# Performance work log

Measured on AMD Instinct MI355X. Metric: run time of the kernel, lower is better.

The kernel has to match this reference:

```python
import jax, jax.numpy as jnp
import numpy as np

N = 50000      # nodes
E = 800000     # edges
T = 3          # npass
ED = 64        # embedding_dim
NS = 23        # nshifts (arange(0.8, 3.0+1e-5, 0.1))
MD = NS + ED   # message_dim = 87
H = 200        # hidden width (hardcoded in module)
NMOL = 2048    # number of molecules (segments for final scatter)
RD = ED * (T + 1)  # readout input dim = 256
EPS = 1e-5

SHIFTS = jnp.asarray(np.arange(0.8, 3.0 + 1e-5, 0.1, dtype=np.float32))  # [23]


def setup_inputs() -> dict:
    key = jax.random.key(0)
    ks = jax.random.split(key, 32)
    inp = {
        'z_i': jax.random.randint(ks[0], (N,), 0, 10),
        'edge_index': jax.random.randint(ks[1], (2, E), 0, N),
        'dist_ij': jax.random.uniform(ks[2], (E, 1), dtype=jnp.float32) * 2.2 + 0.8,
        'mol_ind': jnp.sort(jax.random.randint(ks[3], (N,), 0, NMOL)),
        'emb': jax.random.normal(ks[4], (10, ED), dtype=jnp.float32),
        # per-pass update MLP params, stacked over T
        'up_bn_g': jnp.ones((T, MD), jnp.float32),
        'up_bn_b': jnp.zeros((T, MD), jnp.float32),
        'up_w1': jax.random.normal(ks[5], (T, MD, H), jnp.float32) * 0.05,
        'up_b1': jnp.zeros((T, H), jnp.float32),
        'up_w2': jax.random.normal(ks[6], (T, H, H), jnp.float32) * 0.05,
        'up_b2': jnp.zeros((T, H), jnp.float32),
        'up_w3': jax.random.normal(ks[7], (T, H, H), jnp.float32) * 0.05,
        'up_b3': jnp.zeros((T, H), jnp.float32),
        'up_w4': jax.random.normal(ks[8], (T, H, ED), jnp.float32) * 0.05,
        'up_b4': jnp.zeros((T, ED), jnp.float32),
        # readout MLP params
        'ro_bn_g': jnp.ones((RD,), jnp.float32),
        'ro_bn_b': jnp.zeros((RD,), jnp.float32),
        'ro_w1': jax.random.normal(ks[9], (RD, H), jnp.float32) * 0.05,
        'ro_b1': jnp.zeros((H,), jnp.float32),
        'ro_w2': jax.random.normal(ks[10], (H, H), jnp.float32) * 0.05,
        'ro_b2': jnp.zeros((H,), jnp.float32),
        'ro_w3': jax.random.normal(ks[11], (H, H), jnp.float32) * 0.05,
        'ro_b3': jnp.zeros((H,), jnp.float32),
        'ro_w4': jax.random.normal(ks[12], (H, 1), jnp.float32) * 0.05,
        'ro_b4': jnp.zeros((1,), jnp.float32),  # bias filled to 0 in __init__
    }
    return inp


def batchnorm(x, g, b):
    # BatchNorm1d in training mode: batch statistics, biased variance
    mu = jnp.mean(x, axis=0)
    var = jnp.mean(jnp.square(x - mu), axis=0)
    return (x - mu) * jax.lax.rsqrt(var + EPS) * g + b


def mlp(x, g, b, w1, b1, w2, b2, w3, b3, w4, b4):
    x = batchnorm(x, g, b)
    x = jax.nn.relu(x @ w1 + b1)
    x = jax.nn.relu(x @ w2 + b2)
    x = jax.nn.relu(x @ w3 + b3)
    return x @ w4 + b4


def reference(z_i, edge_index, dist_ij, mol_ind, emb,
              up_bn_g, up_bn_b, up_w1, up_b1, up_w2, up_b2, up_w3, up_b3, up_w4, up_b4,
              ro_bn_g, ro_bn_b, ro_w1, ro_b1, ro_w2, ro_b2, ro_w3, ro_b3, ro_w4, ro_b4):
    e_source, e_sink = edge_index[0], edge_index[1]
    rbf_ij = jnp.exp(-jnp.square(dist_ij - SHIFTS[None, :]))  # [E, NS]
    x_i = emb[z_i]                                            # [N, ED]
    x_list = [x_i]
    for t in range(T):
        m_ij = jnp.concatenate([rbf_ij, x_i[e_sink]], axis=1)  # [E, MD] gather
        m_i = jax.ops.segment_sum(m_ij, e_source, num_segments=N)  # scatter-sum
        x_i = x_i + 0.1 * mlp(m_i, up_bn_g[t], up_bn_b[t],
                              up_w1[t], up_b1[t], up_w2[t], up_b2[t],
                              up_w3[t], up_b3[t], up_w4[t], up_b4[t])
        x_list.append(x_i)
    x_all = jnp.concatenate(x_list, axis=1)  # [N, RD]
    y_i = mlp(x_all, ro_bn_g, ro_bn_b, ro_w1, ro_b1, ro_w2, ro_b2, ro_w3, ro_b3, ro_w4, ro_b4)
    y = jax.ops.segment_sum(y_i, mol_ind, num_segments=NMOL)  # [NMOL, 1]
    return y
```

## Files before the change

### kernel.cpp

```cpp
#include <hip/hip_runtime.h>
#include <hip/hip_bf16.h>
#include <type_traits>

#define NN 50000
#define NP 50048
#define EE 800000
#define TT 3
#define ED 64
#define NS 23
#define MD 87
#define HH 200
#define NMOL 2048
#define RD 256

#define SP 216
#define NPB2 512
#define SNB ((NN + 255) / 256)

typedef __attribute__((ext_vector_type(8))) short short8b;
typedef __attribute__((ext_vector_type(4))) short short4b;
typedef __attribute__((ext_vector_type(4))) float f32x4;

__device__ __forceinline__ unsigned short f2bf(float f) {
  unsigned u = __float_as_uint(f);
  return (unsigned short)((u + 0x7fffu + ((u >> 16) & 1u)) >> 16);
}
__device__ __forceinline__ float ubf2f(unsigned short h) {
  return __uint_as_float(((unsigned)h) << 16);
}
__device__ __forceinline__ float bfp2f(unsigned p) {
  return __uint_as_float(p << 16) + __uint_as_float(p & 0xffff0000u);
}
__device__ __forceinline__ unsigned packsplit(float v) {
  unsigned short h = f2bf(v);
  unsigned short l = f2bf(v - ubf2f(h));
  return (unsigned)h | ((unsigned)l << 16);
}

struct WD { const float* src; short* dst; int K, N, Kpad, Npad, T; };
struct WDs { WD d[5]; };

__global__ __launch_bounds__(256) void wprep_kernel(WDs W) {
  WD w = W.d[blockIdx.y];
  int KB = w.Kpad >> 5, NT = w.Npad >> 4;
  int per = w.Npad * w.Kpad;
  int total = w.T * per;
  for (int idx = blockIdx.x * 256 + threadIdx.x; idx < total; idx += gridDim.x * 256) {
    int t = idx / per;
    int r = idx - t * per;
    int e = r & 7, lane = (r >> 3) & 63;
    int blk = r >> 9;
    int kb = blk % KB, tile = blk / KB;
    int ln = lane & 15, quad = lane >> 4;
    int n = tile * 16 + ln, k = kb * 32 + quad * 8 + e;
    float v = 0.f;
    if (k < w.K && n < w.N) v = w.src[((size_t)t * w.K + k) * w.N + n];
    unsigned short h = f2bf(v);
    unsigned short l = f2bf(v - ubf2f(h));
    size_t base = ((size_t)(t * NT + tile) * KB + kb) * 1024;
    w.dst[base + lane * 8 + e] = (short)h;
    w.dst[base + 512 + lane * 8 + e] = (short)l;
  }
}

__global__ __launch_bounds__(256) void wscale_kernel(const float* __restrict__ wsrc,
                                                     const float* __restrict__ na,
                                                     const float* __restrict__ nb,
                                                     const float* __restrict__ bsrc,
                                                     int K, int Kpad,
                                                     short* __restrict__ wsp,
                                                     float* __restrict__ bc) {
  int n = blockIdx.x;
  int k = threadIdx.x;
  int KB = Kpad >> 5;
  int tile = n >> 4, ln = n & 15;
  float contrib = 0.f;
  if (k < Kpad) {
    float v = 0.f;
    if (n < HH && k < K) {
      float w = wsrc[(size_t)k * HH + n];
      v = na[k] * w;
      contrib = nb[k] * w;
    }
    unsigned short h = f2bf(v);
    unsigned short l = f2bf(v - ubf2f(h));
    int kb = k >> 5, quad = (k & 31) >> 3, e = k & 7;
    int lane = quad * 16 + ln;
    size_t base = ((size_t)tile * KB + kb) * 1024;
    wsp[base + lane * 8 + e] = (short)h;
    wsp[base + 512 + lane * 8 + e] = (short)l;
  }
  __shared__ float sh[256];
  sh[k] = contrib;
  __syncthreads();
  for (int off = 128; off > 0; off >>= 1) {
    if (k < off) sh[k] += sh[k + off];
    __syncthreads();
  }
  if (k == 0) bc[n] = (n < HH ? bsrc[n] : 0.f) + sh[0];
}

__global__ __launch_bounds__(256) void emb_kernel(const int* __restrict__ z,
                                                  const float* __restrict__ emb,
                                                  unsigned* __restrict__ xp,
                                                  short* __restrict__ xq,
                                                  short* __restrict__ xqs) {
  int idx = blockIdx.x * 256 + threadIdx.x;
  if (idx >= NN * ED) return;
  int i = idx >> 6, d = idx & 63;
  unsigned pk = packsplit(emb[z[i] * ED + d]);
  xp[(size_t)i * RD + d] = pk;
  short h = (short)(pk & 0xffffu);
  xq[(size_t)i * RD + d] = h;
  xqs[(size_t)i * ED + d] = h;
}

__global__ __launch_bounds__(256) void hist_kernel(const int* __restrict__ src,
                                                   int* __restrict__ deg) {
  int e = blockIdx.x * 256 + threadIdx.x;
  if (e < EE) atomicAdd(&deg[src[e]], 1);
}

__global__ __launch_bounds__(256) void scanA_kernel(const int* __restrict__ deg,
                                                    int* __restrict__ Psum) {
  int i = blockIdx.x * 256 + threadIdx.x;
  int v = (i < NN) ? deg[i] : 0;
#pragma unroll
  for (int off = 32; off > 0; off >>= 1) v += __shfl_down(v, off, 64);
  __shared__ int ws[4];
  if ((threadIdx.x & 63) == 0) ws[threadIdx.x >> 6] = v;
  __syncthreads();
  if (threadIdx.x == 0) Psum[blockIdx.x] = ws[0] + ws[1] + ws[2] + ws[3];
}

__global__ __launch_bounds__(256) void scanB_kernel(const int* __restrict__ Psum,
                                                    int* __restrict__ Poff) {
  __shared__ int sh[256];
  int t = threadIdx.x;
  int v = (t < SNB) ? Psum[t] : 0;
  sh[t] = v;
  __syncthreads();
  for (int off = 1; off < 256; off <<= 1) {
    int u = (t >= off) ? sh[t - off] : 0;
    __syncthreads();
    sh[t] += u;
    __syncthreads();
  }
  if (t < SNB) Poff[t] = sh[t] - v;
}

__global__ __launch_bounds__(256) void scanC_kernel(const int* __restrict__ deg,
                                                    const int* __restrict__ Poff,
                                                    int* __restrict__ offs,
                                                    int* __restrict__ cursor) {
  __shared__ int sh[256];
  int t = threadIdx.x;
  int i = blockIdx.x * 256 + t;
  int v = (i < NN) ? deg[i] : 0;
  sh[t] = v;
  __syncthreads();
  for (int off = 1; off < 256; off <<= 1) {
    int u = (t >= off) ? sh[t - off] : 0;
    __syncthreads();
    sh[t] += u;
    __syncthreads();
  }
  int excl = Poff[blockIdx.x] + sh[t] - v;
  if (i < NN) {
    offs[i] = excl;
    cursor[i] = excl;
    if (i == NN - 1) offs[NN] = excl + v;
  }
}

__global__ __launch_bounds__(256) void scatter_kernel(const int* __restrict__ src,
                                                      const int* __restrict__ snk,
                                                      const float* __restrict__ dist,
                                                      int* __restrict__ cursor,
                                                      int* __restrict__ ssink,
                                                      float* __restrict__ sdist) {
  int e = blockIdx.x * 256 + threadIdx.x;
  if (e >= EE) return;
  int p = atomicAdd(&cursor[src[e]], 1);
  ssink[p] = snk[e];
  sdist[p] = dist[e];
}

template <bool RBF>
__global__ __launch_bounds__(256) void gather_kernel(const int* __restrict__ offs,
                                                     const int* __restrict__ ssink,
                                                     const float* __restrict__ sdist,
                                                     const short* __restrict__ xqs,
                                                     short* __restrict__ mh) {
  int node = blockIdx.x * 4 + (threadIdx.x >> 6);
  int lane = threadIdx.x & 63;
  if (node >= NN) return;
  float shift = (float)(0.8 + 0.1 * (double)lane);
  int e0 = offs[node], e1 = offs[node + 1];
  float ax0 = 0.f, ax1 = 0.f, ar0 = 0.f, ar1 = 0.f;
  int j = e0;
  for (; j + 4 <= e1; j += 4) {
    int s0 = ssink[j], s1 = ssink[j + 1], s2 = ssink[j + 2], s3 = ssink[j + 3];
    float x0 = ubf2f((unsigned short)xqs[(size_t)s0 * ED + lane]);
    float x1 = ubf2f((unsigned short)xqs[(size_t)s1 * ED + lane]);
    float x2 = ubf2f((unsigned short)xqs[(size_t)s2 * ED + lane]);
    float x3 = ubf2f((unsigned short)xqs[(size_t)s3 * ED + lane]);
    ax0 += x0 + x2;
    ax1 += x1 + x3;
    if (RBF && lane < NS) {
      float d0 = sdist[j], d1 = sdist[j + 1], d2 = sdist[j + 2], d3 = sdist[j + 3];
      float u0 = d0 - shift, u1 = d1 - shift, u2 = d2 - shift, u3 = d3 - shift;
      ar0 += __expf(-u0 * u0) + __expf(-u2 * u2);
      ar1 += __expf(-u1 * u1) + __expf(-u3 * u3);
    }
  }
  for (; j < e1; j++) {
    int s = ssink[j];
    ax0 += ubf2f((unsigned short)xqs[(size_t)s * ED + lane]);
    if (RBF && lane < NS) {
      float u = sdist[j] - shift;
      ar0 += __expf(-u * u);
    }
  }
  float accx = ax0 + ax1;
  if (RBF && lane < NS) mh[(size_t)node * 96 + lane] = (short)f2bf(ar0 + ar1);
  mh[(size_t)node * 96 + NS + lane] = (short)f2bf(accx);
}

template <int LD>
__global__ __launch_bounds__(256) void colstats_s16_kernel(const short* __restrict__ X,
                                                           float* __restrict__ P) {
  constexpr int CG = LD / 8;
  constexpr int RPB = 256 / CG;
  const int t = threadIdx.x;
  const int cg = t % CG, rin = t / CG;
  float s[8] = {0, 0, 0, 0, 0, 0, 0, 0}, q[8] = {0, 0, 0, 0, 0, 0, 0, 0};
  if (rin < RPB) {
    for (int r = blockIdx.x * RPB + rin; r < NN; r += gridDim.x * RPB) {
      union { uint4 v; short e[8]; } u;
      u.v = *(const uint4*)(X + (size_t)r * LD + cg * 8);
#pragma unroll
      for (int e = 0; e < 8; e++) {
        float f = ubf2f((unsigned short)u.e[e]);
        s[e] += f;
        q[e] += f * f;
      }
    }
  }
  __shared__ float sh[256][16];
#pragma unroll
  for (int e = 0; e < 8; e++) { sh[t][e] = s[e]; sh[t][8 + e] = q[e]; }
  __syncthreads();
  if (rin == 0) {
    for (int rr = 1; rr < RPB; rr++) {
      const float* o = sh[rr * CG + cg];
#pragma unroll
      for (int e = 0; e < 8; e++) { s[e] += o[e]; q[e] += o[8 + e]; }
    }
    float* Pb = P + blockIdx.x * 512;
#pragma unroll
    for (int e = 0; e < 8; e++) {
      Pb[cg * 8 + e] = s[e];
      Pb[256 + cg * 8 + e] = q[e];
    }
  }
}

__global__ __launch_bounds__(256) void bnfinal2_kernel(const float* __restrict__ P, int nblk,
                                                       const float* __restrict__ g,
                                                       const float* __restrict__ b, int ncols,
                                                       float* __restrict__ na,
                                                       float* __restrict__ nb) {
  int c = blockIdx.x;
  int t = threadIdx.x;
  float s = 0.f, q = 0.f;
  for (int i = t; i < nblk; i += 256) {
    s += P[i * 512 + c];
    q += P[i * 512 + 256 + c];
  }
#pragma unroll
  for (int off = 32; off > 0; off >>= 1) {
    s += __shfl_down(s, off, 64);
    q += __shfl_down(q, off, 64);
  }
  __shared__ float ws[4], wq[4];
  if ((t & 63) == 0) { ws[t >> 6] = s; wq[t >> 6] = q; }
  __syncthreads();
  if (t == 0) {
    s = ws[0] + ws[1] + ws[2] + ws[3];
    q = wq[0] + wq[1] + wq[2] + wq[3];
    if (c < ncols) {
      float mean = s / (float)NN;
      float var = q / (float)NN - mean * mean;
      float a = g[c] * rsqrtf(var + 1e-5f);
      na[c] = a;
      nb[c] = b[c] - mean * a;
    } else {
      na[c] = 0.f;
      nb[c] = 0.f;
    }
  }
}

template <bool READOUT>
__global__ __launch_bounds__(512, 4) void fused_kernel(
    const short* __restrict__ Agh, int glda,
    const short* __restrict__ W1p, int KB1,
    const short* __restrict__ W2p, const short* __restrict__ W3p,
    const short* __restrict__ W4p,
    const float* __restrict__ b1, const float* __restrict__ b2,
    const float* __restrict__ b3, const float* __restrict__ b4,
    unsigned* __restrict__ xp, short* __restrict__ xq, short* __restrict__ xqs,
    int t, const float* __restrict__ w4ro, const int* __restrict__ mol,
    float* __restrict__ out) {
  __shared__ short ldsH[64 * SP + 16];
  const int tid = threadIdx.x;
  const int wave = tid >> 6, lane = tid & 63, ln = lane & 15, quad = lane >> 4;
  const int bm = blockIdx.x * 64;
  const int ntile = (wave < 5) ? 2 : 1;
  const int tile0 = (wave < 5) ? 2 * wave : wave + 5;
  const int n0col = tile0 * 16;

  if (tid < 16) ldsH[64 * SP + tid] = 0;

  f32x4 acc[4][2];

  auto layer = [&](auto ga_tag, auto terms_tag, const short* __restrict__ Wp,
                   int KB, int KP) {
    constexpr bool GA = decltype(ga_tag)::value;
    constexpr int TERMS = decltype(terms_tag)::value;
#pragma unroll
    for (int i = 0; i < 4; i++)
#pragma unroll
      for (int j = 0; j < 2; j++) acc[i][j] = (f32x4){0.f, 0.f, 0.f, 0.f};
    for (int k0 = 0; k0 < KP; k0 += 32) {
      const int kb = k0 >> 5;
      short8b ah[4], bh[2], bl[2];
#pragma unroll
      for (int i = 0; i < 4; i++) {
        int r = i * 16 + ln;
        if constexpr (GA)
          ah[i] = *(const short8b*)(Agh + (size_t)(bm + r) * glda + k0 + quad * 8);
        else
          ah[i] = *(const short8b*)(ldsH + r * SP + k0 + quad * 8);
      }
#pragma unroll
      for (int j = 0; j < 2; j++)
        if (j < ntile) {
          const short* bp = Wp + ((size_t)((tile0 + j) * KB + kb)) * 1024 + lane * 8;
          bh[j] = *(const short8b*)bp;
          if constexpr (TERMS == 2) bl[j] = *(const short8b*)(bp + 512);
        }
#pragma unroll
      for (int j = 0; j < 2; j++)
        if (j < ntile)
#pragma unroll
          for (int i = 0; i < 4; i++) {
            acc[i][j] = __builtin_amdgcn_mfma_f32_16x16x32_bf16(ah[i], bh[j], acc[i][j], 0, 0, 0);
            if constexpr (TERMS == 2)
              acc[i][j] =
                  __builtin_amdgcn_mfma_f32_16x16x32_bf16(ah[i], bl[j], acc[i][j], 0, 0, 0);
          }
    }
  };

  auto epi = [&](const float* __restrict__ bias) {
    __syncthreads();
#pragma unroll
    for (int i = 0; i < 4; i++)
#pragma unroll
      for (int j = 0; j < 2; j++)
        if (j < ntile)
#pragma unroll
          for (int r = 0; r < 4; r++) {
            int row = i * 16 + quad * 4 + r;
            int col = n0col + j * 16 + ln;
            float v = acc[i][j][r] + (col < HH ? bias[col] : 0.f);
            v = fmaxf(v, 0.f);
            ldsH[row * SP + col] = (short)f2bf(v);
          }
    ldsH[(tid >> 3) * SP + 208 + (tid & 7)] = 0;
    __syncthreads();
  };

  using one_t = std::integral_constant<int, 1>;
  using two_t = std::integral_constant<int, 2>;

  if (!READOUT) {
    layer(std::true_type{}, two_t{}, W1p, KB1, 96);
    epi(b1);
    layer(std::false_type{}, one_t{}, W2p, 7, 224);
    epi(b2);
    layer(std::false_type{}, one_t{}, W3p, 7, 224);
    epi(b3);
    const int wm4 = wave & 1, wn4 = wave >> 1;
    f32x4 a4[2];
#pragma unroll
    for (int i = 0; i < 2; i++) a4[i] = (f32x4){0.f, 0.f, 0.f, 0.f};
    for (int k0 = 0; k0 < 224; k0 += 32) {
      const int kb = k0 >> 5;
      short8b ah[2], bh, bl;
#pragma unroll
      for (int i = 0; i < 2; i++) {
        int r = wm4 * 32 + i * 16 + ln;
        ah[i] = *(const short8b*)(ldsH + r * SP + k0 + quad * 8);
      }
      const short* bp = W4p + ((size_t)(wn4 * 7 + kb)) * 1024 + lane * 8;
      bh = *(const short8b*)bp;
      bl = *(const short8b*)(bp + 512);
#pragma unroll
      for (int i = 0; i < 2; i++) {
        a4[i] = __builtin_amdgcn_mfma_f32_16x16x32_bf16(ah[i], bh, a4[i], 0, 0, 0);
        a4[i] = __builtin_amdgcn_mfma_f32_16x16x32_bf16(ah[i], bl, a4[i], 0, 0, 0);
      }
    }
#pragma unroll
    for (int i = 0; i < 2; i++)
#pragma unroll
      for (int r = 0; r < 4; r++) {
        int grow = bm + wm4 * 32 + i * 16 + quad * 4 + r;
        int col = wn4 * 16 + ln;
        if (grow < NN) {
          float v = a4[i][r] + b4[col];
          size_t base = (size_t)grow * RD;
          float old = bfp2f(xp[base + (size_t)t * ED + col]);
          unsigned pk = packsplit(old + 0.1f * v);
          xp[base + (size_t)(t + 1) * ED + col] = pk;
          short h = (short)(pk & 0xffffu);
          xq[base + (size_t)(t + 1) * ED + col] = h;
          xqs[(size_t)(t + 1) * NN * ED + (size_t)grow * ED + col] = h;
        }
      }
  } else {
    layer(std::true_type{}, two_t{}, W1p, KB1, 256);
    epi(b1);
    layer(std::false_type{}, one_t{}, W2p, 7, 224);
    epi(b2);
    layer(std::false_type{}, one_t{}, W3p, 7, 224);
    epi(b3);
    int row = tid >> 3;
    int grow = bm + row;
    float s = 0.f;
    for (int c = (tid & 7); c < HH; c += 8)
      s += ubf2f((unsigned short)ldsH[row * SP + c]) * w4ro[c];
    s += __shfl_xor(s, 1, 64);
    s += __shfl_xor(s, 2, 64);
    s += __shfl_xor(s, 4, 64);
    if ((tid & 7) == 0 && grow < NN) atomicAdd(&out[mol[grow]], s + b4[0]);
  }
}

extern "C" void kernel_launch(void* const* d_in, const int* in_sizes, int n_in,
                              void* d_out, int out_size, void* d_ws, size_t ws_size,
                              hipStream_t stream) {
  const int* z_i = (const int*)d_in[0];
  const int* e_src = (const int*)d_in[1];
  const int* e_snk = ((const int*)d_in[1]) + EE;
  const float* dist = (const float*)d_in[2];
  const int* mol = (const int*)d_in[3];
  const float* emb = (const float*)d_in[4];
  const float* up_bn_g = (const float*)d_in[5];
  const float* up_bn_b = (const float*)d_in[6];
  const float* up_w1 = (const float*)d_in[7];
  const float* up_b1 = (const float*)d_in[8];
  const float* up_w2 = (const float*)d_in[9];
  const float* up_b2 = (const float*)d_in[10];
  const float* up_w3 = (const float*)d_in[11];
  const float* up_b3 = (const float*)d_in[12];
  const float* up_w4 = (const float*)d_in[13];
  const float* up_b4 = (const float*)d_in[14];
  const float* ro_bn_g = (const float*)d_in[15];
  const float* ro_bn_b = (const float*)d_in[16];
  const float* ro_w1 = (const float*)d_in[17];
  const float* ro_b1 = (const float*)d_in[18];
  const float* ro_w2 = (const float*)d_in[19];
  const float* ro_b2 = (const float*)d_in[20];
  const float* ro_w3 = (const float*)d_in[21];
  const float* ro_b3 = (const float*)d_in[22];
  const float* ro_w4 = (const float*)d_in[23];
  const float* ro_b4 = (const float*)d_in[24];
  float* out = (float*)d_out;

  char* p = (char*)d_ws;
  auto alloc = [&](size_t bytes) {
    void* r = (void*)p;
    p += (bytes + 255) & ~(size_t)255;
    return r;
  };
  unsigned* x_p = (unsigned*)alloc((size_t)NN * RD * 4);
  short* x_q = (short*)alloc((size_t)NP * RD * 2);
  short* x_qs = (short*)alloc((size_t)(TT + 1) * NN * ED * 2);
  short* mh = (short*)alloc((size_t)NP * 96 * 2);
  int* ssink = (int*)alloc((size_t)EE * 4);
  float* sdist = (float*)alloc((size_t)EE * 4);
  int* offs = (int*)alloc((size_t)(NN + 1) * 4);
  int* deg = (int*)alloc((size_t)NN * 4);
  int* cursor = (int*)alloc((size_t)NN * 4);
  int* Psum = (int*)alloc((size_t)SNB * 4);
  int* Poff = (int*)alloc((size_t)SNB * 4);
  float* P = (float*)alloc((size_t)NPB2 * 512 * 4);
  float* na = (float*)alloc(256 * 4);
  float* nb = (float*)alloc(256 * 4);
  float* b1c = (float*)alloc(208 * 4);
  short* w1sp = (short*)alloc((size_t)13 * 3 * 1024 * 2);
  short* r1sp = (short*)alloc((size_t)13 * 8 * 1024 * 2);
  short* w2p = (short*)alloc((size_t)TT * 13 * 7 * 1024 * 2);
  short* w3p = (short*)alloc((size_t)TT * 13 * 7 * 1024 * 2);
  short* w4p = (short*)alloc((size_t)TT * 4 * 7 * 1024 * 2);
  short* r2p = (short*)alloc((size_t)13 * 7 * 1024 * 2);
  short* r3p = (short*)alloc((size_t)13 * 7 * 1024 * 2);

  hipMemsetAsync(deg, 0, (size_t)NN * 4, stream);
  hipMemsetAsync(out, 0, (size_t)NMOL * 4, stream);

  WDs descs;
  descs.d[0] = {up_w2, w2p, HH, HH, 224, 208, TT};
  descs.d[1] = {up_w3, w3p, HH, HH, 224, 208, TT};
  descs.d[2] = {up_w4, w4p, HH, ED, 224, 64, TT};
  descs.d[3] = {ro_w2, r2p, HH, HH, 224, 208, 1};
  descs.d[4] = {ro_w3, r3p, HH, HH, 224, 208, 1};
  wprep_kernel<<<dim3(546, 5), 256, 0, stream>>>(descs);

  emb_kernel<<<(NN * ED + 255) / 256, 256, 0, stream>>>(z_i, emb, x_p, x_q, x_qs);
  hist_kernel<<<(EE + 255) / 256, 256, 0, stream>>>(e_src, deg);
  scanA_kernel<<<SNB, 256, 0, stream>>>(deg, Psum);
  scanB_kernel<<<1, 256, 0, stream>>>(Psum, Poff);
  scanC_kernel<<<SNB, 256, 0, stream>>>(deg, Poff, offs, cursor);
  scatter_kernel<<<(EE + 255) / 256, 256, 0, stream>>>(e_src, e_snk, dist, cursor, ssink, sdist);

  const int gM = NP / 64;

  for (int t = 0; t < TT; t++) {
    if (t == 0)
      gather_kernel<true><<<(NN + 3) / 4, 256, 0, stream>>>(
          offs, ssink, sdist, x_qs, mh);
    else
      gather_kernel<false><<<(NN + 3) / 4, 256, 0, stream>>>(
          offs, ssink, sdist, x_qs + (size_t)t * NN * ED, mh);
    colstats_s16_kernel<96><<<NPB2, 256, 0, stream>>>(mh, P);
    bnfinal2_kernel<<<256, 256, 0, stream>>>(P, NPB2, up_bn_g + t * MD, up_bn_b + t * MD, MD,
                                             na, nb);
    wscale_kernel<<<208, 256, 0, stream>>>(up_w1 + (size_t)t * MD * HH, na, nb,
                                           up_b1 + t * HH, MD, 96, w1sp, b1c);
    fused_kernel<false><<<gM, 512, 0, stream>>>(
        mh, 96, w1sp, 3,
        w2p + (size_t)t * 13 * 7 * 1024, w3p + (size_t)t * 13 * 7 * 1024,
        w4p + (size_t)t * 4 * 7 * 1024,
        b1c, up_b2 + t * HH, up_b3 + t * HH, up_b4 + t * ED,
        x_p, x_q, x_qs, t, nullptr, nullptr, nullptr);
  }

  colstats_s16_kernel<256><<<NPB2, 256, 0, stream>>>(x_q, P);
  bnfinal2_kernel<<<256, 256, 0, stream>>>(P, NPB2, ro_bn_g, ro_bn_b, RD, na, nb);
  wscale_kernel<<<208, 256, 0, stream>>>(ro_w1, na, nb, ro_b1, RD, 256, r1sp, b1c);
  fused_kernel<true><<<gM, 512, 0, stream>>>(
      x_q, 256, r1sp, 8,
      r2p, r3p, nullptr,
      b1c, ro_b2, ro_b3, ro_b4,
      nullptr, nullptr, nullptr, 0, ro_w4, mol, out);

  (void)in_sizes; (void)n_in; (void)out_size; (void)ws_size;
}
```

Baseline: 610.5 us.

## Restructure fused MLP kernel so each wave owns 16 rows across all columns

The fused MLP kernel now uses 256-thread blocks where each wave processes its own 16-row slice through all four layers, keeping A fragments in registers and storing intermediates in a private per-wave LDS slab. This removes the block-wide __syncthreads between layers and the repeated LDS reads of A across column tiles. The cost is that each wave re-reads every weight tile from global/L2 (less weight reuse per row) and uses more registers for the held A fragments. The gather kernel also zeroes the padding columns of the message buffer so the K-padded first layer reads defined data.

```diff
diff --git a/kernel.cpp b/kernel.cpp
--- a/kernel.cpp
+++ b/kernel.cpp
@@ -13,13 +13,14 @@
 #define NMOL 2048
 #define RD 256
 
-#define SP 216
+#define SW 232
 #define NPB2 512
 #define SNB ((NN + 255) / 256)
 
 typedef __attribute__((ext_vector_type(8))) short short8b;
-typedef __attribute__((ext_vector_type(4))) short short4b;
 typedef __attribute__((ext_vector_type(4))) float f32x4;
+
+template <int V> using ic = std::integral_constant<int, V>;
 
 __device__ __forceinline__ unsigned short f2bf(float f) {
   unsigned u = __float_as_uint(f);
@@ -224,6 +225,7 @@
   }
   float accx = ax0 + ax1;
   if (RBF && lane < NS) mh[(size_t)node * 96 + lane] = (short)f2bf(ar0 + ar1);
+  if (RBF && lane >= NS && lane < 32) mh[(size_t)node * 96 + 64 + lane] = 0;
   mh[(size_t)node * 96 + NS + lane] = (short)f2bf(accx);
 }
 
@@ -303,150 +305,134 @@
 }
 
 template <bool READOUT>
-__global__ __launch_bounds__(512, 4) void fused_kernel(
-    const short* __restrict__ Agh, int glda,
-    const short* __restrict__ W1p, int KB1,
-    const short* __restrict__ W2p, const short* __restrict__ W3p,
-    const short* __restrict__ W4p,
+__global__ __launch_bounds__(256, 4) void fused_kernel(
+    const short* __restrict__ Agh,
+    const short* __restrict__ W1p, const short* __restrict__ W2p,
+    const short* __restrict__ W3p, const short* __restrict__ W4p,
     const float* __restrict__ b1, const float* __restrict__ b2,
     const float* __restrict__ b3, const float* __restrict__ b4,
     unsigned* __restrict__ xp, short* __restrict__ xq, short* __restrict__ xqs,
     int t, const float* __restrict__ w4ro, const int* __restrict__ mol,
     float* __restrict__ out) {
-  __shared__ short ldsH[64 * SP + 16];
+  __shared__ short lds[4 * 16 * SW];
+  constexpr int GLDA = READOUT ? RD : 96;
+  constexpr int KB1 = READOUT ? 8 : 3;
   const int tid = threadIdx.x;
   const int wave = tid >> 6, lane = tid & 63, ln = lane & 15, quad = lane >> 4;
-  const int bm = blockIdx.x * 64;
-  const int ntile = (wave < 5) ? 2 : 1;
-  const int tile0 = (wave < 5) ? 2 * wave : wave + 5;
-  const int n0col = tile0 * 16;
-
-  if (tid < 16) ldsH[64 * SP + tid] = 0;
-
-  f32x4 acc[4][2];
-
-  auto layer = [&](auto ga_tag, auto terms_tag, const short* __restrict__ Wp,
-                   int KB, int KP) {
-    constexpr bool GA = decltype(ga_tag)::value;
-    constexpr int TERMS = decltype(terms_tag)::value;
-#pragma unroll
-    for (int i = 0; i < 4; i++)
-#pragma unroll
-      for (int j = 0; j < 2; j++) acc[i][j] = (f32x4){0.f, 0.f, 0.f, 0.f};
-    for (int k0 = 0; k0 < KP; k0 += 32) {
-      const int kb = k0 >> 5;
-      short8b ah[4], bh[2], bl[2];
-#pragma unroll
-      for (int i = 0; i < 4; i++) {
-        int r = i * 16 + ln;
-        if constexpr (GA)
-          ah[i] = *(const short8b*)(Agh + (size_t)(bm + r) * glda + k0 + quad * 8);
-        else
-          ah[i] = *(const short8b*)(ldsH + r * SP + k0 + quad * 8);
-      }
-#pragma unroll
-      for (int j = 0; j < 2; j++)
-        if (j < ntile) {
-          const short* bp = Wp + ((size_t)((tile0 + j) * KB + kb)) * 1024 + lane * 8;
-          bh[j] = *(const short8b*)bp;
-          if constexpr (TERMS == 2) bl[j] = *(const short8b*)(bp + 512);
+  const int q8 = quad * 8;
+  const int bm = (blockIdx.x * 4 + wave) * 16;
+  short* ldsW = lds + wave * (16 * SW);
+  const short* aRow = ldsW + ln * SW;
+
+#pragma unroll
+  for (int p = 0; p < 6; p++) {
+    int idx = p * 64 + lane;
+    ldsW[(idx / 24) * SW + 208 + (idx % 24)] = 0;
+  }
+
+  f32x4 acc[2];
+  auto pair = [&](auto kbt, auto tt, const short8b* a, const short* __restrict__ Wp,
+                  int j0, int nj) {
+    constexpr int KB = decltype(kbt)::value;
+    constexpr int TERMS = decltype(tt)::value;
+#pragma unroll
+    for (int jj = 0; jj < 2; jj++) acc[jj] = (f32x4){0.f, 0.f, 0.f, 0.f};
+#pragma unroll
+    for (int kb = 0; kb < KB; kb++)
+#pragma unroll
+      for (int jj = 0; jj < 2; jj++)
+        if (jj < nj) {
+          const short* bp = Wp + (size_t)((j0 + jj) * KB + kb) * 1024 + lane * 8;
+          acc[jj] = __builtin_amdgcn_mfma_f32_16x16x32_bf16(a[kb], *(const short8b*)bp,
+                                                            acc[jj], 0, 0, 0);
+          if constexpr (TERMS == 2)
+            acc[jj] = __builtin_amdgcn_mfma_f32_16x16x32_bf16(
+                a[kb], *(const short8b*)(bp + 512), acc[jj], 0, 0, 0);
         }
-#pragma unroll
-      for (int j = 0; j < 2; j++)
-        if (j < ntile)
-#pragma unroll
-          for (int i = 0; i < 4; i++) {
-            acc[i][j] = __builtin_amdgcn_mfma_f32_16x16x32_bf16(ah[i], bh[j], acc[i][j], 0, 0, 0);
-            if constexpr (TERMS == 2)
-              acc[i][j] =
-                  __builtin_amdgcn_mfma_f32_16x16x32_bf16(ah[i], bl[j], acc[i][j], 0, 0, 0);
+  };
+  auto epi = [&](int j, const f32x4& ac, const float* __restrict__ bias) {
+    int colg = j * 16 + ln;
+    float bb = (colg < HH) ? bias[colg] : 0.f;
+#pragma unroll
+    for (int r = 0; r < 4; r++)
+      ldsW[(quad * 4 + r) * SW + colg] = (short)f2bf(fmaxf(ac[r] + bb, 0.f));
+  };
+
+  {
+    short8b a1[KB1];
+#pragma unroll
+    for (int kb = 0; kb < KB1; kb++)
+      a1[kb] = *(const short8b*)(Agh + (size_t)(bm + ln) * GLDA + kb * 32 + q8);
+#pragma unroll
+    for (int j0 = 0; j0 < 13; j0 += 2) {
+      int nj = (13 - j0 >= 2) ? 2 : 1;
+      pair(ic<KB1>{}, ic<2>{}, a1, W1p, j0, nj);
+      epi(j0, acc[0], b1);
+      if (nj == 2) epi(j0 + 1, acc[1], b1);
+    }
+  }
+  short8b a[7];
+#pragma unroll
+  for (int kb = 0; kb < 7; kb++)
+    a[kb] = *(const short8b*)(aRow + kb * 32 + q8);
+
+#pragma unroll
+  for (int j0 = 0; j0 < 13; j0 += 2) {
+    int nj = (13 - j0 >= 2) ? 2 : 1;
+    pair(ic<7>{}, ic<1>{}, a, W2p, j0, nj);
+    epi(j0, acc[0], b2);
+    if (nj == 2) epi(j0 + 1, acc[1], b2);
+  }
+#pragma unroll
+  for (int kb = 0; kb < 7; kb++)
+    a[kb] = *(const short8b*)(aRow + kb * 32 + q8);
+
+#pragma unroll
+  for (int j0 = 0; j0 < 13; j0 += 2) {
+    int nj = (13 - j0 >= 2) ? 2 : 1;
+    pair(ic<7>{}, ic<1>{}, a, W3p, j0, nj);
+    epi(j0, acc[0], b3);
+    if (nj == 2) epi(j0 + 1, acc[1], b3);
+  }
+#pragma unroll
+  for (int kb = 0; kb < 7; kb++)
+    a[kb] = *(const short8b*)(aRow + kb * 32 + q8);
+
+  if constexpr (!READOUT) {
+#pragma unroll
+    for (int j0 = 0; j0 < 4; j0 += 2) {
+      pair(ic<7>{}, ic<2>{}, a, W4p, j0, 2);
+#pragma unroll
+      for (int jj = 0; jj < 2; jj++) {
+        int colg = (j0 + jj) * 16 + ln;
+        float bb = b4[colg];
+#pragma unroll
+        for (int r = 0; r < 4; r++) {
+          int grow = bm + quad * 4 + r;
+          if (grow < NN) {
+            size_t base = (size_t)grow * RD;
+            float oldv = bfp2f(xp[base + (size_t)t * ED + colg]);
+            unsigned pk = packsplit(oldv + 0.1f * (acc[jj][r] + bb));
+            xp[base + (size_t)(t + 1) * ED + colg] = pk;
+            short h = (short)(pk & 0xffffu);
+            xq[base + (size_t)(t + 1) * ED + colg] = h;
+            xqs[(size_t)(t + 1) * NN * ED + (size_t)grow * ED + colg] = h;
           }
-    }
-  };
-
-  auto epi = [&](const float* __restrict__ bias) {
-    __syncthreads();
-#pragma unroll
-    for (int i = 0; i < 4; i++)
-#pragma unroll
-      for (int j = 0; j < 2; j++)
-        if (j < ntile)
-#pragma unroll
-          for (int r = 0; r < 4; r++) {
-            int row = i * 16 + quad * 4 + r;
-            int col = n0col + j * 16 + ln;
-            float v = acc[i][j][r] + (col < HH ? bias[col] : 0.f);
-            v = fmaxf(v, 0.f);
-            ldsH[row * SP + col] = (short)f2bf(v);
-          }
-    ldsH[(tid >> 3) * SP + 208 + (tid & 7)] = 0;
-    __syncthreads();
-  };
-
-  using one_t = std::integral_constant<int, 1>;
-  using two_t = std::integral_constant<int, 2>;
-
-  if (!READOUT) {
-    layer(std::true_type{}, two_t{}, W1p, KB1, 96);
-    epi(b1);
-    layer(std::false_type{}, one_t{}, W2p, 7, 224);
-    epi(b2);
-    layer(std::false_type{}, one_t{}, W3p, 7, 224);
-    epi(b3);
-    const int wm4 = wave & 1, wn4 = wave >> 1;
-    f32x4 a4[2];
-#pragma unroll
-    for (int i = 0; i < 2; i++) a4[i] = (f32x4){0.f, 0.f, 0.f, 0.f};
-    for (int k0 = 0; k0 < 224; k0 += 32) {
-      const int kb = k0 >> 5;
-      short8b ah[2], bh, bl;
-#pragma unroll
-      for (int i = 0; i < 2; i++) {
-        int r = wm4 * 32 + i * 16 + ln;
-        ah[i] = *(const short8b*)(ldsH + r * SP + k0 + quad * 8);
-      }
-      const short* bp = W4p + ((size_t)(wn4 * 7 + kb)) * 1024 + lane * 8;
-      bh = *(const short8b*)bp;
-      bl = *(const short8b*)(bp + 512);
-#pragma unroll
-      for (int i = 0; i < 2; i++) {
-        a4[i] = __builtin_amdgcn_mfma_f32_16x16x32_bf16(ah[i], bh, a4[i], 0, 0, 0);
-        a4[i] = __builtin_amdgcn_mfma_f32_16x16x32_bf16(ah[i], bl, a4[i], 0, 0, 0);
-      }
-    }
-#pragma unroll
-    for (int i = 0; i < 2; i++)
-#pragma unroll
-      for (int r = 0; r < 4; r++) {
-        int grow = bm + wm4 * 32 + i * 16 + quad * 4 + r;
-        int col = wn4 * 16 + ln;
-        if (grow < NN) {
-          float v = a4[i][r] + b4[col];
-          size_t base = (size_t)grow * RD;
-          float old = bfp2f(xp[base + (size_t)t * ED + col]);
-          unsigned pk = packsplit(old + 0.1f * v);
-          xp[base + (size_t)(t + 1) * ED + col] = pk;
-          short h = (short)(pk & 0xffffu);
-          xq[base + (size_t)(t + 1) * ED + col] = h;
-          xqs[(size_t)(t + 1) * NN * ED + (size_t)grow * ED + col] = h;
         }
       }
+    }
   } else {
-    layer(std::true_type{}, two_t{}, W1p, KB1, 256);
-    epi(b1);
-    layer(std::false_type{}, one_t{}, W2p, 7, 224);
-    epi(b2);
-    layer(std::false_type{}, one_t{}, W3p, 7, 224);
-    epi(b3);
-    int row = tid >> 3;
-    int grow = bm + row;
     float s = 0.f;
-    for (int c = (tid & 7); c < HH; c += 8)
-      s += ubf2f((unsigned short)ldsH[row * SP + c]) * w4ro[c];
-    s += __shfl_xor(s, 1, 64);
-    s += __shfl_xor(s, 2, 64);
-    s += __shfl_xor(s, 4, 64);
-    if ((tid & 7) == 0 && grow < NN) atomicAdd(&out[mol[grow]], s + b4[0]);
+#pragma unroll
+    for (int kb = 0; kb < 7; kb++)
+      if (kb * 32 + q8 < HH)
+#pragma unroll
+        for (int e = 0; e < 8; e++)
+          s += ubf2f((unsigned short)a[kb][e]) * w4ro[kb * 32 + q8 + e];
+    s += __shfl_xor(s, 16, 64);
+    s += __shfl_xor(s, 32, 64);
+    int grow = bm + ln;
+    if (lane < 16 && grow < NN) atomicAdd(&out[mol[grow]], s + b4[0]);
   }
 }
 
@@ -542,8 +528,8 @@
                                              na, nb);
     wscale_kernel<<<208, 256, 0, stream>>>(up_w1 + (size_t)t * MD * HH, na, nb,
                                            up_b1 + t * HH, MD, 96, w1sp, b1c);
-    fused_kernel<false><<<gM, 512, 0, stream>>>(
-        mh, 96, w1sp, 3,
+    fused_kernel<false><<<gM, 256, 0, stream>>>(
+        mh, w1sp,
         w2p + (size_t)t * 13 * 7 * 1024, w3p + (size_t)t * 13 * 7 * 1024,
         w4p + (size_t)t * 4 * 7 * 1024,
         b1c, up_b2 + t * HH, up_b3 + t * HH, up_b4 + t * ED,
@@ -553,9 +539,8 @@
   colstats_s16_kernel<256><<<NPB2, 256, 0, stream>>>(x_q, P);
   bnfinal2_kernel<<<256, 256, 0, stream>>>(P, NPB2, ro_bn_g, ro_bn_b, RD, na, nb);
   wscale_kernel<<<208, 256, 0, stream>>>(ro_w1, na, nb, ro_b1, RD, 256, r1sp, b1c);
-  fused_kernel<true><<<gM, 512, 0, stream>>>(
-      x_q, 256, r1sp, 8,
-      r2p, r3p, nullptr,
+  fused_kernel<true><<<gM, 256, 0, stream>>>(
+      x_q, r1sp, r2p, r3p, nullptr,
       b1c, ro_b2, ro_b3, ro_b4,
       nullptr, nullptr, nullptr, 0, ro_w4, mol, out);
 
```

After: 606.7 us. No clear change (-0.6%).
